# Optimization experiments

Hardware: AMD Instinct MI355X
Metric: run time of the kernel (lower is better)

## Reference

```python
import jax, jax.numpy as jnp
import numpy as np

STRIDE, PAD, DIL = 1, 1, 1


def setup_inputs() -> dict:
    key = jax.random.key(0)
    ks = jax.random.split(key, 5)
    N, Cin, H, W = 8, 256, 56, 56
    Cout, kh, kw = 256, 3, 3
    x = jax.random.normal(ks[0], (N, Cin, H, W), jnp.float32)
    offset = jax.random.normal(ks[1], (N, 2 * kh * kw, H, W), jnp.float32)
    mask = jax.random.uniform(ks[2], (N, kh * kw, H, W), jnp.float32)
    fan_in = Cin * kh * kw
    bound = float(np.sqrt(6.0 / fan_in))  # kaiming_uniform, relu gain
    weight = jax.random.uniform(ks[3], (Cout, Cin, kh, kw), jnp.float32, -bound, bound)
    bias = jnp.zeros((Cout,), jnp.float32)
    return {"x": x, "offset": offset, "mask": mask, "weight": weight, "bias": bias}


def _mdcn(x, offset, mask, weight, bias):
    N, Cin, H, W = x.shape
    Cout, _, kh, kw = weight.shape
    K = kh * kw
    Hout = (H + 2 * PAD - (DIL * (kh - 1) + 1)) // STRIDE + 1
    Wout = (W + 2 * PAD - (DIL * (kw - 1) + 1)) // STRIDE + 1
    # offset channels: [K, 2(y,x)] interleaved -> [N,K,2,Hout,Wout]
    off = offset.reshape(N, K, 2, Hout, Wout)
    dy, dx = off[:, :, 0], off[:, :, 1]
    ky = (jnp.arange(K) // kw) * DIL
    kx = (jnp.arange(K) % kw) * DIL
    base_y = jnp.arange(Hout) * STRIDE - PAD
    base_x = jnp.arange(Wout) * STRIDE - PAD
    py = dy + ky[None, :, None, None] + base_y[None, None, :, None]  # [N,K,Ho,Wo]
    px = dx + kx[None, :, None, None] + base_x[None, None, None, :]
    y0 = jnp.floor(py)
    x0 = jnp.floor(px)
    wy1 = py - y0
    wx1 = px - x0
    wy0 = 1.0 - wy1
    wx0 = 1.0 - wx1
    y0i = y0.astype(jnp.int32)
    x0i = x0.astype(jnp.int32)
    x_nhwc = jnp.transpose(x, (0, 2, 3, 1))  # [N,H,W,Cin]
    nidx = jnp.arange(N)[:, None, None, None]

    def gather(yi, xi):
        valid = (yi >= 0) & (yi < H) & (xi >= 0) & (xi < W)
        yc = jnp.clip(yi, 0, H - 1)
        xc = jnp.clip(xi, 0, W - 1)
        v = x_nhwc[nidx, yc, xc]  # [N,K,Ho,Wo,Cin]
        return v * valid[..., None].astype(x.dtype)

    v = (gather(y0i, x0i) * (wy0 * wx0)[..., None]
         + gather(y0i, x0i + 1) * (wy0 * wx1)[..., None]
         + gather(y0i + 1, x0i) * (wy1 * wx0)[..., None]
         + gather(y0i + 1, x0i + 1) * (wy1 * wx1)[..., None])
    v = v * mask.reshape(N, K, Hout, Wout)[..., None]
    wr = weight.reshape(Cout, Cin, K)
    out = jnp.einsum('nkhwc,ock->nohw', v, wr)
    return out + bias[None, :, None, None]


def reference(x, offset, mask, weight, bias):
    return _mdcn(x, offset, mask, weight, bias)
```

## Files before the change

### kernel.cpp

```cpp
#include <hip/hip_runtime.h>
#include <math.h>

#define H_ 56
#define W_ 56
#define CIN 256
#define COUT 256
#define NB 8
#define SPIX 3136
#define KG 2304
#define MTOT 25088
#define MT 128
#define NBLK 196
#define GUARD_PX 2048

typedef _Float16 v8hf __attribute__((ext_vector_type(8)));
typedef float    v4f  __attribute__((ext_vector_type(4)));

#define WAIT_VM(N)  do { asm volatile("s_waitcnt vmcnt(" #N ")" ::: "memory"); \
                         __builtin_amdgcn_sched_barrier(0); } while (0)
#define WAIT_LGKM0  do { asm volatile("s_waitcnt lgkmcnt(0)" ::: "memory"); \
                         __builtin_amdgcn_sched_barrier(0); } while (0)
#define BARR        do { asm volatile("s_barrier" ::: "memory"); } while (0)

__device__ __forceinline__ void async_copy16(const void* g, void* l) {
    __builtin_amdgcn_global_load_lds(
        (const __attribute__((address_space(1))) void*)g,
        (__attribute__((address_space(3))) void*)l, 16, 0, 0);
}

__global__ __launch_bounds__(256) void prep_xw(const float* __restrict__ x,
                                               const float* __restrict__ w,
                                               _Float16* __restrict__ xb,
                                               _Float16* __restrict__ bp) {
    __shared__ float tile[64][65];
    const int tid = threadIdx.x;
    if (blockIdx.z < 8) {
        const int n = blockIdx.z, c0 = blockIdx.y * 64, s0 = blockIdx.x * 64;
        const float* xp = x + (size_t)n * CIN * SPIX;
        _Float16* xo = xb + (size_t)n * SPIX * CIN;
#pragma unroll
        for (int i = 0; i < 16; ++i) {
            int idx = tid + i * 256;
            int cr = idx >> 6, sc = idx & 63;
            tile[cr][sc] = xp[(c0 + cr) * SPIX + s0 + sc];
        }
        __syncthreads();
#pragma unroll
        for (int i = 0; i < 16; ++i) {
            int idx = tid + i * 256;
            int sr = idx >> 6, cc = idx & 63;
            xo[(s0 + sr) * CIN + c0 + cc] = (_Float16)tile[cc][sr];
        }
    } else if (blockIdx.z == 8) {
        const int base = (blockIdx.y * 49 + blockIdx.x) * 256 + tid;
        for (int i = base; i < COUT * KG; i += 196 * 256) {
            const int o = i / KG;
            const int rem = i - o * KG;
            const int c = rem / 9;
            const int tap = rem - c * 9;
            bp[(size_t)o * KG + tap * 256 + c] = (_Float16)w[i];
        }
    } else {
        const int gtid = (blockIdx.y * 49 + blockIdx.x) * 256 + tid;
        v8hf* lo = (v8hf*)(xb - (size_t)GUARD_PX * CIN);
        v8hf* hi = (v8hf*)(xb + (size_t)NB * SPIX * CIN);
        const v8hf z = (v8hf)(_Float16)0.f;
        for (int i = gtid; i < 65536; i += 196 * 256) {
            lo[i] = z;
            hi[i] = z;
        }
    }
}

__device__ __forceinline__ void compute_params(
    const float* __restrict__ offs, const float* __restrict__ msk,
    int m0, int* sS, float4* sW, int tid)
{
    for (int idx = tid; idx < 9 * MT; idx += 512) {
        const int tl = idx >> 7, pl = idx & 127;
        const int pg = m0 + pl;
        const int n  = pg / SPIX;
        const int s  = pg - n * SPIX;
        const int h  = s / W_, w = s - h * W_;
        const int kY = tl / 3, kX = tl - kY * 3;
        const float dy = offs[n * (18 * SPIX) + (2 * tl) * SPIX + s];
        const float dx = offs[n * (18 * SPIX) + (2 * tl + 1) * SPIX + s];
        const float mk = msk[n * (9 * SPIX) + tl * SPIX + s];
        const float py = dy + (float)(kY + h - 1);
        const float px = dx + (float)(kX + w - 1);
        const float fy0 = floorf(py), fx0 = floorf(px);
        const int y0 = (int)fy0, x0 = (int)fx0;
        const float wy1 = py - fy0, wx1 = px - fx0;
        const float wy0 = 1.f - wy1, wx0 = 1.f - wx1;
        const bool yv0 = (y0 >= 0) & (y0 < H_);
        const bool yv1 = (y0 + 1 >= 0) & (y0 + 1 < H_);
        const bool xv0 = (x0 >= 0) & (x0 < W_);
        const bool xv1 = (x0 + 1 >= 0) & (x0 + 1 < W_);
        float4 wt;
        wt.x = (yv0 & xv0) ? wy0 * wx0 * mk : 0.f;
        wt.y = (yv0 & xv1) ? wy0 * wx1 * mk : 0.f;
        wt.z = (yv1 & xv0) ? wy1 * wx0 * mk : 0.f;
        wt.w = (yv1 & xv1) ? wy1 * wx1 * mk : 0.f;
        int base = n * SPIX + y0 * W_ + x0;
        base = min(max(base, -GUARD_PX), NB * SPIX - 58 + GUARD_PX);
        sS[idx] = base * CIN;
        sW[idx] = wt;
    }
}

__global__ __launch_bounds__(512, 2) void mdcn_fused6(
    const _Float16* __restrict__ xb,
    const float*    __restrict__ offs,
    const float*    __restrict__ msk,
    const _Float16* __restrict__ bp,
    const float*    __restrict__ bias,
    float*          __restrict__ out)
{
    __shared__ __align__(16) char smem[121344];
    int*    sS = (int*)(smem + 98304);
    float4* sW = (float4*)(smem + 102912);

    const int tid  = threadIdx.x;
    const int lane = tid & 63, wv = tid >> 6;
    const int wm = wv & 1, wn = wv >> 1;
    const int l15 = lane & 15, q = lane >> 4;

    const int xcd = blockIdx.x & 7, ib = blockIdx.x >> 3;
    const int wg  = (xcd < 4) ? xcd * 25 + ib : 100 + (xcd - 4) * 24 + ib;
    const int m0  = wg * MT;

    compute_params(offs, msk, m0, sS, sW, tid);

    v4f acc[4][4];
#pragma unroll
    for (int i = 0; i < 4; ++i)
#pragma unroll
        for (int j = 0; j < 4; ++j) acc[i][j] = (v4f)0.f;

    __syncthreads();

    const int pxl = tid >> 2, c2 = tid & 3;
    v8hf ga0, ga1, ga2, ga3, gb0, gb1, gb2, gb3;
    float4 cw;
    v8hf afr[2][4], bfr[2][4];

#define GATHER(E, KQ)                                                   \
    { const int b_ = sS[E] + ((KQ) << 6) + c2 * 8;                      \
      cw  = sW[E];                                                      \
      ga0 = *(const v8hf*)(xb + b_);                                    \
      ga1 = *(const v8hf*)(xb + b_ + 256);                              \
      ga2 = *(const v8hf*)(xb + b_ + 14336);                            \
      ga3 = *(const v8hf*)(xb + b_ + 14592);                            \
      gb0 = *(const v8hf*)(xb + b_ + 32);                               \
      gb1 = *(const v8hf*)(xb + b_ + 288);                              \
      gb2 = *(const v8hf*)(xb + b_ + 14368);                            \
      gb3 = *(const v8hf*)(xb + b_ + 14624); }

#define COMBINE_STORE(AP)                                               \
    { const _Float16 wx_ = (_Float16)cw.x, wy_ = (_Float16)cw.y;        \
      const _Float16 wz_ = (_Float16)cw.z, ww_ = (_Float16)cw.w;        \
      v8hf r0_ = ga0 * wx_ + ga1 * wy_ + ga2 * wz_ + ga3 * ww_;         \
      v8hf r1_ = gb0 * wx_ + gb1 * wy_ + gb2 * wz_ + gb3 * ww_;         \
      *(v8hf*)((AP) + pxl * 64 + (((c2)     ^ (pxl & 7)) << 3)) = r0_;  \
      *(v8hf*)((AP) + pxl * 64 + (((c2 + 4) ^ (pxl & 7)) << 3)) = r1_; }

#define STAGE_B(K0, LB)                                                 \
    do { _Pragma("unroll")                                              \
      for (int t = 0; t < 4; ++t) {                                     \
        const int brow = t * 64 + (wv << 3) + (lane >> 3);              \
        const int blc  = (lane & 7) ^ (brow & 7);                       \
        async_copy16(bp + (size_t)brow * KG + (K0) + blc * 8,           \
                     (LB) + ((t * 8 + wv) << 10)); } } while (0)

#define LOAD_FRAGS(AB, BB)                                              \
    { _Pragma("unroll")                                                 \
      for (int kf = 0; kf < 2; ++kf) {                                  \
        _Pragma("unroll")                                               \
        for (int mt = 0; mt < 4; ++mt) {                                \
          const int row = wm * 64 + mt * 16 + l15;                      \
          const int pch = (kf * 4 + q) ^ (row & 7);                     \
          afr[kf][mt] = *(const v8hf*)((_Float16*)(AB) + row * 64 + pch * 8); } \
        _Pragma("unroll")                                               \
        for (int nt = 0; nt < 4; ++nt) {                                \
          const int row = wn * 64 + nt * 16 + l15;                      \
          const int pch = (kf * 4 + q) ^ (row & 7);                     \
          bfr[kf][nt] = *(const v8hf*)((_Float16*)(BB) + row * 64 + pch * 8); } } }

#define MFMA_EXEC                                                       \
    { __builtin_amdgcn_s_setprio(1);                                    \
      _Pragma("unroll")                                                 \
      for (int kf = 0; kf < 2; ++kf)                                    \
        _Pragma("unroll")                                               \
        for (int mt = 0; mt < 4; ++mt)                                  \
          _Pragma("unroll")                                             \
          for (int nt = 0; nt < 4; ++nt)                                \
            acc[mt][nt] = __builtin_amdgcn_mfma_f32_16x16x32_f16(       \
                afr[kf][mt], bfr[kf][nt], acc[mt][nt], 0, 0, 0);        \
      __builtin_amdgcn_s_setprio(0); }

    GATHER(pxl, 0)
    COMBINE_STORE((_Float16*)smem)
    STAGE_B(0, smem + 32768);
    GATHER(pxl, 1)
    WAIT_LGKM0;
    WAIT_VM(8);
    BARR;

    char* ac = smem;          char* an = smem + 16384;
    char* bc = smem + 32768;  char* bn = smem + 65536;

#pragma unroll 1
    for (int ks = 0; ks < 36; ++ks) {
        LOAD_FRAGS(ac, bc);
        if (ks < 35) {
            STAGE_B((ks + 1) << 6, bn);
            WAIT_VM(4);
            COMBINE_STORE((_Float16*)an)
            if (ks < 34) {
                const int st = ks + 2;
                GATHER((st >> 2) * MT + pxl, st & 3)
            }
        }

        MFMA_EXEC;

        if (ks < 34) {
            WAIT_LGKM0;
            WAIT_VM(8);
            BARR;
        } else if (ks == 34) {
            WAIT_LGKM0;
            WAIT_VM(0);
            BARR;
        }
        char* t;
        t = ac; ac = an; an = t;
        t = bc; bc = bn; bn = t;
    }
#undef GATHER
#undef COMBINE_STORE
#undef STAGE_B
#undef LOAD_FRAGS
#undef MFMA_EXEC

    WAIT_LGKM0;
    BARR;
    float* epi = (float*)smem + wv * 1104;
    const int pg_l = m0 + wm * 64 + lane;
    const int n_l  = pg_l / SPIX;
    float* outp = out + (size_t)n_l * (COUT * SPIX) + (pg_l - n_l * SPIX);

#pragma unroll
    for (int nt = 0; nt < 4; ++nt) {
        const float bv = bias[wn * 64 + nt * 16 + l15];
#pragma unroll
        for (int mt = 0; mt < 4; ++mt)
#pragma unroll
            for (int r = 0; r < 4; ++r)
                epi[(mt * 16 + q * 4 + r) * 17 + l15] = acc[mt][nt][r] + bv;
#pragma unroll
        for (int oc = 0; oc < 16; ++oc)
            outp[(size_t)(wn * 64 + nt * 16 + oc) * SPIX] = epi[lane * 17 + oc];
    }
}

#define BM 64
#define BN 64
#define BKF 32
#define AST 68
#define BST 68
#define CST 65
__global__ __launch_bounds__(256) void mdcn_fallback(
    const float* __restrict__ xs, const float* __restrict__ offs,
    const float* __restrict__ msk, const float* __restrict__ wraw,
    const float* __restrict__ bias, float* __restrict__ out)
{
    __shared__ float smem[BKF * AST + BKF * BST];
    __shared__ int   sBase[4][BM];
    __shared__ float sWgt[4][BM];
    float (*At)[AST] = (float (*)[AST])smem;
    float (*Bt)[BST] = (float (*)[BST])(smem + BKF * AST);
    float (*Cs)[CST] = (float (*)[CST])smem;
    const int tid = threadIdx.x;
    const int m0 = blockIdx.x * BM;
    const int o0 = blockIdx.y * BN;
    const int n  = m0 / SPIX;
    const int s0 = m0 - n * SPIX;
    const int tx = tid & 15, ty = tid >> 4;
    float acc[4][4] = {};
    for (int k = 0; k < 9; ++k) {
        if (tid < BM) {
            const int s = s0 + tid;
            const int h = s / W_;
            const int w = s - h * W_;
            const int kY = k / 3, kX = k - kY * 3;
            const float dy = offs[(size_t)n * (18 * SPIX) + (size_t)(2 * k) * SPIX + s];
            const float dx = offs[(size_t)n * (18 * SPIX) + (size_t)(2 * k + 1) * SPIX + s];
            const float mk = msk[(size_t)n * (9 * SPIX) + (size_t)k * SPIX + s];
            const float py = dy + (float)(kY + h - 1);
            const float px = dx + (float)(kX + w - 1);
            const float fy0 = floorf(py), fx0 = floorf(px);
            const int y0 = (int)fy0, x0 = (int)fx0;
            const float wy1 = py - fy0, wx1 = px - fx0;
            const float wy0 = 1.0f - wy1, wx0 = 1.0f - wx1;
#pragma unroll
            for (int t = 0; t < 4; ++t) {
                const int yi = y0 + (t >> 1), xi = x0 + (t & 1);
                const bool valid = (yi >= 0) & (yi < H_) & (xi >= 0) & (xi < W_);
                const int yc = min(max(yi, 0), H_ - 1);
                const int xc = min(max(xi, 0), W_ - 1);
                float wt = ((t >> 1) ? wy1 : wy0) * ((t & 1) ? wx1 : wx0) * mk;
                sBase[t][tid] = n * (CIN * SPIX) + yc * W_ + xc;
                sWgt[t][tid] = valid ? wt : 0.0f;
            }
        }
        __syncthreads();
        for (int c0 = 0; c0 < CIN; c0 += BKF) {
#pragma unroll
            for (int i = 0; i < 8; ++i) {
                int idx = tid + i * 256;
                int row = idx >> 5, cc = idx & 31;
                int ce = (c0 + cc) * SPIX;
                At[cc][row] = sWgt[0][row] * xs[sBase[0][row] + ce]
                            + sWgt[1][row] * xs[sBase[1][row] + ce]
                            + sWgt[2][row] * xs[sBase[2][row] + ce]
                            + sWgt[3][row] * xs[sBase[3][row] + ce];
            }
#pragma unroll
            for (int i = 0; i < 8; ++i) {
                int idx = tid + i * 256;
                int kf = idx >> 6, o = idx & 63;
                Bt[kf][o] = wraw[(size_t)(o0 + o) * KG + (c0 + kf) * 9 + k];
            }
            __syncthreads();
#pragma unroll
            for (int kf = 0; kf < BKF; ++kf) {
                const float4 a = *(const float4*)&At[kf][ty * 4];
                const float4 b = *(const float4*)&Bt[kf][tx * 4];
                acc[0][0] = fmaf(a.x, b.x, acc[0][0]); acc[0][1] = fmaf(a.x, b.y, acc[0][1]);
                acc[0][2] = fmaf(a.x, b.z, acc[0][2]); acc[0][3] = fmaf(a.x, b.w, acc[0][3]);
                acc[1][0] = fmaf(a.y, b.x, acc[1][0]); acc[1][1] = fmaf(a.y, b.y, acc[1][1]);
                acc[1][2] = fmaf(a.y, b.z, acc[1][2]); acc[1][3] = fmaf(a.y, b.w, acc[1][3]);
                acc[2][0] = fmaf(a.z, b.x, acc[2][0]); acc[2][1] = fmaf(a.z, b.y, acc[2][1]);
                acc[2][2] = fmaf(a.z, b.z, acc[2][2]); acc[2][3] = fmaf(a.z, b.w, acc[2][3]);
                acc[3][0] = fmaf(a.w, b.x, acc[3][0]); acc[3][1] = fmaf(a.w, b.y, acc[3][1]);
                acc[3][2] = fmaf(a.w, b.z, acc[3][2]); acc[3][3] = fmaf(a.w, b.w, acc[3][3]);
            }
            __syncthreads();
        }
    }
#pragma unroll
    for (int i = 0; i < 4; ++i)
#pragma unroll
        for (int j = 0; j < 4; ++j)
            Cs[ty * 4 + i][tx * 4 + j] = acc[i][j] + bias[o0 + tx * 4 + j];
    __syncthreads();
    const int pix = tid & 63, ob = tid >> 6;
    float* outp = out + (size_t)n * COUT * SPIX + s0 + pix;
#pragma unroll
    for (int r = 0; r < 16; ++r) {
        int o = r * 4 + ob;
        outp[(size_t)(o0 + o) * SPIX] = Cs[pix][o];
    }
}

extern "C" void kernel_launch(void* const* d_in, const int* in_sizes, int n_in,
                              void* d_out, int out_size, void* d_ws, size_t ws_size,
                              hipStream_t stream) {
    const float* x    = (const float*)d_in[0];
    const float* offs = (const float*)d_in[1];
    const float* msk  = (const float*)d_in[2];
    const float* w    = (const float*)d_in[3];
    const float* bias = (const float*)d_in[4];
    float* out = (float*)d_out;

    const size_t GUARD_B  = (size_t)GUARD_PX * CIN * sizeof(_Float16);
    const size_t xb_bytes = (size_t)NB * SPIX * CIN * sizeof(_Float16);
    const size_t bp_bytes = (size_t)KG * COUT * sizeof(_Float16);
    const size_t need     = GUARD_B + xb_bytes + GUARD_B + bp_bytes;

    if (ws_size >= need) {
        _Float16* xb = (_Float16*)((char*)d_ws + GUARD_B);
        _Float16* bp = (_Float16*)((char*)d_ws + GUARD_B + xb_bytes + GUARD_B);
        prep_xw<<<dim3(49, 4, 10), 256, 0, stream>>>(x, w, xb, bp);
        mdcn_fused6<<<dim3(NBLK), 512, 0, stream>>>(xb, offs, msk, bp, bias, out);
    } else {
        mdcn_fallback<<<dim3(MTOT / BM, COUT / BN), 256, 0, stream>>>(
            x, offs, msk, w, bias, out);
    }
}
```

Before: 143.3 us.

## Halve M tile, stream B fragments directly into registers, drop LDS B staging

The fused kernel moves from 128-pixel tiles with 512 threads to 64-pixel tiles with 256 threads and 392 blocks, which shrinks LDS from about 121KB to about 28KB. Each wave now owns 64 output channels and loads its B (weight) fragments straight from global memory into double-buffered registers, replacing the async global-to-LDS copies and the LDS fragment reads. The main loop is unrolled by two to alternate the A and B buffers. This aims for more blocks in flight and less LDS traffic, at the cost of each block re-reading the full weight matrix from global/L2 and more register pressure.

```diff
diff --git a/kernel.cpp b/kernel.cpp
--- a/kernel.cpp
+++ b/kernel.cpp
@@ -9,8 +9,8 @@
 #define SPIX 3136
 #define KG 2304
 #define MTOT 25088
-#define MT 128
-#define NBLK 196
+#define MT 64
+#define NBLK2 392
 #define GUARD_PX 2048
 
 typedef _Float16 v8hf __attribute__((ext_vector_type(8)));
@@ -21,12 +21,6 @@
 #define WAIT_LGKM0  do { asm volatile("s_waitcnt lgkmcnt(0)" ::: "memory"); \
                          __builtin_amdgcn_sched_barrier(0); } while (0)
 #define BARR        do { asm volatile("s_barrier" ::: "memory"); } while (0)
-
-__device__ __forceinline__ void async_copy16(const void* g, void* l) {
-    __builtin_amdgcn_global_load_lds(
-        (const __attribute__((address_space(1))) void*)g,
-        (__attribute__((address_space(3))) void*)l, 16, 0, 0);
-}
 
 __global__ __launch_bounds__(256) void prep_xw(const float* __restrict__ x,
                                                const float* __restrict__ w,
@@ -76,8 +70,8 @@
     const float* __restrict__ offs, const float* __restrict__ msk,
     int m0, int* sS, float4* sW, int tid)
 {
-    for (int idx = tid; idx < 9 * MT; idx += 512) {
-        const int tl = idx >> 7, pl = idx & 127;
+    for (int idx = tid; idx < 9 * MT; idx += 256) {
+        const int tl = idx >> 6, pl = idx & 63;
         const int pg = m0 + pl;
         const int n  = pg / SPIX;
         const int s  = pg - n * SPIX;
@@ -108,7 +102,7 @@
     }
 }
 
-__global__ __launch_bounds__(512, 2) void mdcn_fused6(
+__global__ __launch_bounds__(256, 2) void mdcn_fused8(
     const _Float16* __restrict__ xb,
     const float*    __restrict__ offs,
     const float*    __restrict__ msk,
@@ -116,18 +110,18 @@
     const float*    __restrict__ bias,
     float*          __restrict__ out)
 {
-    __shared__ __align__(16) char smem[121344];
-    int*    sS = (int*)(smem + 98304);
-    float4* sW = (float4*)(smem + 102912);
+    __shared__ __align__(16) char smem[28160];
+    _Float16* A0 = (_Float16*)smem;
+    _Float16* A1 = (_Float16*)(smem + 8192);
+    int*      sS = (int*)(smem + 16384);
+    float4*   sW = (float4*)(smem + 18688);
 
     const int tid  = threadIdx.x;
     const int lane = tid & 63, wv = tid >> 6;
-    const int wm = wv & 1, wn = wv >> 1;
     const int l15 = lane & 15, q = lane >> 4;
 
-    const int xcd = blockIdx.x & 7, ib = blockIdx.x >> 3;
-    const int wg  = (xcd < 4) ? xcd * 25 + ib : 100 + (xcd - 4) * 24 + ib;
-    const int m0  = wg * MT;
+    const int wg = (blockIdx.x & 7) * 49 + (blockIdx.x >> 3);
+    const int m0 = wg * MT;
 
     compute_params(offs, msk, m0, sS, sW, tid);
 
@@ -142,11 +136,13 @@
     const int pxl = tid >> 2, c2 = tid & 3;
     v8hf ga0, ga1, ga2, ga3, gb0, gb1, gb2, gb3;
     float4 cw;
-    v8hf afr[2][4], bfr[2][4];
+    v8hf afr[2][4];
+    v8hf B0r[8], B1r[8];
 
 #define GATHER(E, KQ)                                                   \
-    { const int b_ = sS[E] + ((KQ) << 6) + c2 * 8;                      \
-      cw  = sW[E];                                                      \
+    { const int e_ = (E);                                               \
+      const int b_ = sS[e_] + ((KQ) << 6) + c2 * 8;                     \
+      cw  = sW[e_];                                                     \
       ga0 = *(const v8hf*)(xb + b_);                                    \
       ga1 = *(const v8hf*)(xb + b_ + 256);                              \
       ga2 = *(const v8hf*)(xb + b_ + 14336);                            \
@@ -164,29 +160,24 @@
       *(v8hf*)((AP) + pxl * 64 + (((c2)     ^ (pxl & 7)) << 3)) = r0_;  \
       *(v8hf*)((AP) + pxl * 64 + (((c2 + 4) ^ (pxl & 7)) << 3)) = r1_; }
 
-#define STAGE_B(K0, LB)                                                 \
-    do { _Pragma("unroll")                                              \
-      for (int t = 0; t < 4; ++t) {                                     \
-        const int brow = t * 64 + (wv << 3) + (lane >> 3);              \
-        const int blc  = (lane & 7) ^ (brow & 7);                       \
-        async_copy16(bp + (size_t)brow * KG + (K0) + blc * 8,           \
-                     (LB) + ((t * 8 + wv) << 10)); } } while (0)
-
-#define LOAD_FRAGS(AB, BB)                                              \
+#define ISSUE_B(KS, BR)                                                 \
     { _Pragma("unroll")                                                 \
-      for (int kf = 0; kf < 2; ++kf) {                                  \
+      for (int i = 0; i < 8; ++i) {                                     \
+        const int kf_ = i >> 2, nt_ = i & 3;                            \
+        BR[i] = *(const v8hf*)(bp                                       \
+            + (size_t)(wv * 64 + nt_ * 16 + l15) * KG                   \
+            + (KS) * 64 + (kf_ * 4 + q) * 8); } }
+
+#define LOAD_AFR(AB)                                                    \
+    { _Pragma("unroll")                                                 \
+      for (int kf = 0; kf < 2; ++kf)                                    \
         _Pragma("unroll")                                               \
         for (int mt = 0; mt < 4; ++mt) {                                \
-          const int row = wm * 64 + mt * 16 + l15;                      \
+          const int row = mt * 16 + l15;                                \
           const int pch = (kf * 4 + q) ^ (row & 7);                     \
-          afr[kf][mt] = *(const v8hf*)((_Float16*)(AB) + row * 64 + pch * 8); } \
-        _Pragma("unroll")                                               \
-        for (int nt = 0; nt < 4; ++nt) {                                \
-          const int row = wn * 64 + nt * 16 + l15;                      \
-          const int pch = (kf * 4 + q) ^ (row & 7);                     \
-          bfr[kf][nt] = *(const v8hf*)((_Float16*)(BB) + row * 64 + pch * 8); } } }
-
-#define MFMA_EXEC                                                       \
+          afr[kf][mt] = *(const v8hf*)((AB) + row * 64 + pch * 8); } }
+
+#define MFMA_EXEC(BR)                                                   \
     { __builtin_amdgcn_s_setprio(1);                                    \
       _Pragma("unroll")                                                 \
       for (int kf = 0; kf < 2; ++kf)                                    \
@@ -195,64 +186,69 @@
           _Pragma("unroll")                                             \
           for (int nt = 0; nt < 4; ++nt)                                \
             acc[mt][nt] = __builtin_amdgcn_mfma_f32_16x16x32_f16(       \
-                afr[kf][mt], bfr[kf][nt], acc[mt][nt], 0, 0, 0);        \
+                afr[kf][mt], BR[kf * 4 + nt], acc[mt][nt], 0, 0, 0);    \
       __builtin_amdgcn_s_setprio(0); }
 
+    ISSUE_B(0, B0r);
     GATHER(pxl, 0)
-    COMBINE_STORE((_Float16*)smem)
-    STAGE_B(0, smem + 32768);
+    WAIT_VM(0);
+    COMBINE_STORE(A0)
     GATHER(pxl, 1)
+    ISSUE_B(1, B1r);
     WAIT_LGKM0;
+    BARR;
+
+#pragma unroll 1
+    for (int k2 = 0; k2 < 17; ++k2) {
+        const int e = k2 * 2;
+        LOAD_AFR(A0);
+        WAIT_VM(8);
+        COMBINE_STORE(A1)
+        GATHER(((e + 2) >> 2) * MT + pxl, (e + 2) & 3)
+        WAIT_VM(8);
+        MFMA_EXEC(B0r);
+        ISSUE_B(e + 2, B0r);
+        WAIT_LGKM0;
+        BARR;
+
+        const int o = e + 1;
+        LOAD_AFR(A1);
+        WAIT_VM(8);
+        COMBINE_STORE(A0)
+        GATHER(((o + 2) >> 2) * MT + pxl, (o + 2) & 3)
+        WAIT_VM(8);
+        MFMA_EXEC(B1r);
+        ISSUE_B(o + 2, B1r);
+        WAIT_LGKM0;
+        BARR;
+    }
+
+    LOAD_AFR(A0);
     WAIT_VM(8);
+    COMBINE_STORE(A1)
+    WAIT_VM(0);
+    MFMA_EXEC(B0r);
+    WAIT_LGKM0;
     BARR;
-
-    char* ac = smem;          char* an = smem + 16384;
-    char* bc = smem + 32768;  char* bn = smem + 65536;
-
-#pragma unroll 1
-    for (int ks = 0; ks < 36; ++ks) {
-        LOAD_FRAGS(ac, bc);
-        if (ks < 35) {
-            STAGE_B((ks + 1) << 6, bn);
-            WAIT_VM(4);
-            COMBINE_STORE((_Float16*)an)
-            if (ks < 34) {
-                const int st = ks + 2;
-                GATHER((st >> 2) * MT + pxl, st & 3)
-            }
-        }
-
-        MFMA_EXEC;
-
-        if (ks < 34) {
-            WAIT_LGKM0;
-            WAIT_VM(8);
-            BARR;
-        } else if (ks == 34) {
-            WAIT_LGKM0;
-            WAIT_VM(0);
-            BARR;
-        }
-        char* t;
-        t = ac; ac = an; an = t;
-        t = bc; bc = bn; bn = t;
-    }
+    LOAD_AFR(A1);
+    MFMA_EXEC(B1r);
+
 #undef GATHER
 #undef COMBINE_STORE
-#undef STAGE_B
-#undef LOAD_FRAGS
+#undef ISSUE_B
+#undef LOAD_AFR
 #undef MFMA_EXEC
 
     WAIT_LGKM0;
     BARR;
     float* epi = (float*)smem + wv * 1104;
-    const int pg_l = m0 + wm * 64 + lane;
+    const int pg_l = m0 + lane;
     const int n_l  = pg_l / SPIX;
     float* outp = out + (size_t)n_l * (COUT * SPIX) + (pg_l - n_l * SPIX);
 
 #pragma unroll
     for (int nt = 0; nt < 4; ++nt) {
-        const float bv = bias[wn * 64 + nt * 16 + l15];
+        const float bv = bias[wv * 64 + nt * 16 + l15];
 #pragma unroll
         for (int mt = 0; mt < 4; ++mt)
 #pragma unroll
@@ -260,7 +256,7 @@
                 epi[(mt * 16 + q * 4 + r) * 17 + l15] = acc[mt][nt][r] + bv;
 #pragma unroll
         for (int oc = 0; oc < 16; ++oc)
-            outp[(size_t)(wn * 64 + nt * 16 + oc) * SPIX] = epi[lane * 17 + oc];
+            outp[(size_t)(wv * 64 + nt * 16 + oc) * SPIX] = epi[lane * 17 + oc];
     }
 }
 
@@ -383,7 +379,7 @@
         _Float16* xb = (_Float16*)((char*)d_ws + GUARD_B);
         _Float16* bp = (_Float16*)((char*)d_ws + GUARD_B + xb_bytes + GUARD_B);
         prep_xw<<<dim3(49, 4, 10), 256, 0, stream>>>(x, w, xb, bp);
-        mdcn_fused6<<<dim3(NBLK), 512, 0, stream>>>(xb, offs, msk, bp, bias, out);
+        mdcn_fused8<<<dim3(NBLK2), 256, 0, stream>>>(xb, offs, msk, bp, bias, out);
     } else {
         mdcn_fallback<<<dim3(MTOT / BM, COUT / BN), 256, 0, stream>>>(
             x, offs, msk, w, bias, out);
```

Measured after the change: 171.8 us. 1.2x slower.

## Warp-specialize fused deformable conv into producer gather and consumer MFMA waves

Applied to the files above, without the earlier changes.

Splits the 8 waves of each block into 4 producer waves, which gather the bilinear samples, combine them, and stage weight tiles into LDS, and 4 consumer waves that run only the MFMA loop. Each consumer wave now covers a 64x128 output tile instead of 64x64. The aim is to overlap the irregular gather latency with tensor-core math rather than interleaving both in every wave. In exchange, each producer wave issues twice as many gather loads, consumer waves hold twice as many accumulator registers, and MFMA throughput per block is limited to half the waves.

```diff
diff --git a/kernel.cpp b/kernel.cpp
--- a/kernel.cpp
+++ b/kernel.cpp
@@ -108,7 +108,7 @@
     }
 }
 
-__global__ __launch_bounds__(512, 2) void mdcn_fused6(
+__global__ __launch_bounds__(512, 2) void mdcn_fused9(
     const _Float16* __restrict__ xb,
     const float*    __restrict__ offs,
     const float*    __restrict__ msk,
@@ -122,7 +122,6 @@
 
     const int tid  = threadIdx.x;
     const int lane = tid & 63, wv = tid >> 6;
-    const int wm = wv & 1, wn = wv >> 1;
     const int l15 = lane & 15, q = lane >> 4;
 
     const int xcd = blockIdx.x & 7, ib = blockIdx.x >> 3;
@@ -130,137 +129,158 @@
     const int m0  = wg * MT;
 
     compute_params(offs, msk, m0, sS, sW, tid);
-
-    v4f acc[4][4];
-#pragma unroll
-    for (int i = 0; i < 4; ++i)
-#pragma unroll
-        for (int j = 0; j < 4; ++j) acc[i][j] = (v4f)0.f;
-
     __syncthreads();
 
-    const int pxl = tid >> 2, c2 = tid & 3;
-    v8hf ga0, ga1, ga2, ga3, gb0, gb1, gb2, gb3;
-    float4 cw;
-    v8hf afr[2][4], bfr[2][4];
-
-#define GATHER(E, KQ)                                                   \
-    { const int b_ = sS[E] + ((KQ) << 6) + c2 * 8;                      \
-      cw  = sW[E];                                                      \
-      ga0 = *(const v8hf*)(xb + b_);                                    \
-      ga1 = *(const v8hf*)(xb + b_ + 256);                              \
-      ga2 = *(const v8hf*)(xb + b_ + 14336);                            \
-      ga3 = *(const v8hf*)(xb + b_ + 14592);                            \
-      gb0 = *(const v8hf*)(xb + b_ + 32);                               \
-      gb1 = *(const v8hf*)(xb + b_ + 288);                              \
-      gb2 = *(const v8hf*)(xb + b_ + 14368);                            \
-      gb3 = *(const v8hf*)(xb + b_ + 14624); }
-
-#define COMBINE_STORE(AP)                                               \
-    { const _Float16 wx_ = (_Float16)cw.x, wy_ = (_Float16)cw.y;        \
-      const _Float16 wz_ = (_Float16)cw.z, ww_ = (_Float16)cw.w;        \
-      v8hf r0_ = ga0 * wx_ + ga1 * wy_ + ga2 * wz_ + ga3 * ww_;         \
-      v8hf r1_ = gb0 * wx_ + gb1 * wy_ + gb2 * wz_ + gb3 * ww_;         \
-      *(v8hf*)((AP) + pxl * 64 + (((c2)     ^ (pxl & 7)) << 3)) = r0_;  \
-      *(v8hf*)((AP) + pxl * 64 + (((c2 + 4) ^ (pxl & 7)) << 3)) = r1_; }
-
-#define STAGE_B(K0, LB)                                                 \
-    do { _Pragma("unroll")                                              \
-      for (int t = 0; t < 4; ++t) {                                     \
-        const int brow = t * 64 + (wv << 3) + (lane >> 3);              \
-        const int blc  = (lane & 7) ^ (brow & 7);                       \
-        async_copy16(bp + (size_t)brow * KG + (K0) + blc * 8,           \
-                     (LB) + ((t * 8 + wv) << 10)); } } while (0)
-
-#define LOAD_FRAGS(AB, BB)                                              \
-    { _Pragma("unroll")                                                 \
-      for (int kf = 0; kf < 2; ++kf) {                                  \
-        _Pragma("unroll")                                               \
-        for (int mt = 0; mt < 4; ++mt) {                                \
-          const int row = wm * 64 + mt * 16 + l15;                      \
-          const int pch = (kf * 4 + q) ^ (row & 7);                     \
-          afr[kf][mt] = *(const v8hf*)((_Float16*)(AB) + row * 64 + pch * 8); } \
-        _Pragma("unroll")                                               \
-        for (int nt = 0; nt < 4; ++nt) {                                \
-          const int row = wn * 64 + nt * 16 + l15;                      \
-          const int pch = (kf * 4 + q) ^ (row & 7);                     \
-          bfr[kf][nt] = *(const v8hf*)((_Float16*)(BB) + row * 64 + pch * 8); } } }
-
-#define MFMA_EXEC                                                       \
-    { __builtin_amdgcn_s_setprio(1);                                    \
-      _Pragma("unroll")                                                 \
-      for (int kf = 0; kf < 2; ++kf)                                    \
-        _Pragma("unroll")                                               \
-        for (int mt = 0; mt < 4; ++mt)                                  \
-          _Pragma("unroll")                                             \
-          for (int nt = 0; nt < 4; ++nt)                                \
-            acc[mt][nt] = __builtin_amdgcn_mfma_f32_16x16x32_f16(       \
-                afr[kf][mt], bfr[kf][nt], acc[mt][nt], 0, 0, 0);        \
-      __builtin_amdgcn_s_setprio(0); }
-
-    GATHER(pxl, 0)
-    COMBINE_STORE((_Float16*)smem)
-    STAGE_B(0, smem + 32768);
-    GATHER(pxl, 1)
-    WAIT_LGKM0;
-    WAIT_VM(8);
-    BARR;
-
-    char* ac = smem;          char* an = smem + 16384;
-    char* bc = smem + 32768;  char* bn = smem + 65536;
-
+    if (wv < 4) {
+        const int p2 = tid >> 2, c2 = tid & 3;
+        v8hf gA[8], gB[8];
+        float4 cwA, cwB;
+
+#define GATHER16(TAP, KQ)                                               \
+        { const int e0_ = (TAP) * MT + p2;                              \
+          const int b0_ = sS[e0_]      + ((KQ) << 6) + c2 * 8;          \
+          const int b1_ = sS[e0_ + 64] + ((KQ) << 6) + c2 * 8;          \
+          cwA = sW[e0_]; cwB = sW[e0_ + 64];                            \
+          gA[0] = *(const v8hf*)(xb + b0_);                             \
+          gA[1] = *(const v8hf*)(xb + b0_ + 256);                       \
+          gA[2] = *(const v8hf*)(xb + b0_ + 14336);                     \
+          gA[3] = *(const v8hf*)(xb + b0_ + 14592);                     \
+          gA[4] = *(const v8hf*)(xb + b0_ + 32);                        \
+          gA[5] = *(const v8hf*)(xb + b0_ + 288);                       \
+          gA[6] = *(const v8hf*)(xb + b0_ + 14368);                     \
+          gA[7] = *(const v8hf*)(xb + b0_ + 14624);                     \
+          gB[0] = *(const v8hf*)(xb + b1_);                             \
+          gB[1] = *(const v8hf*)(xb + b1_ + 256);                       \
+          gB[2] = *(const v8hf*)(xb + b1_ + 14336);                     \
+          gB[3] = *(const v8hf*)(xb + b1_ + 14592);                     \
+          gB[4] = *(const v8hf*)(xb + b1_ + 32);                        \
+          gB[5] = *(const v8hf*)(xb + b1_ + 288);                       \
+          gB[6] = *(const v8hf*)(xb + b1_ + 14368);                     \
+          gB[7] = *(const v8hf*)(xb + b1_ + 14624); }
+
+#define COMBINE16(AP)                                                   \
+        { const _Float16 ax_ = (_Float16)cwA.x, ay_ = (_Float16)cwA.y;  \
+          const _Float16 az_ = (_Float16)cwA.z, aw_ = (_Float16)cwA.w;  \
+          const _Float16 bx_ = (_Float16)cwB.x, by_ = (_Float16)cwB.y;  \
+          const _Float16 bz_ = (_Float16)cwB.z, bw_ = (_Float16)cwB.w;  \
+          v8hf rA0 = gA[0]*ax_ + gA[1]*ay_ + gA[2]*az_ + gA[3]*aw_;     \
+          v8hf rA1 = gA[4]*ax_ + gA[5]*ay_ + gA[6]*az_ + gA[7]*aw_;     \
+          v8hf rB0 = gB[0]*bx_ + gB[1]*by_ + gB[2]*bz_ + gB[3]*bw_;     \
+          v8hf rB1 = gB[4]*bx_ + gB[5]*by_ + gB[6]*bz_ + gB[7]*bw_;     \
+          _Float16* ap_ = (_Float16*)(AP);                              \
+          *(v8hf*)(ap_ + p2 * 64        + (((c2)     ^ (p2 & 7)) << 3)) = rA0; \
+          *(v8hf*)(ap_ + p2 * 64        + (((c2 + 4) ^ (p2 & 7)) << 3)) = rA1; \
+          *(v8hf*)(ap_ + (p2 + 64) * 64 + (((c2)     ^ (p2 & 7)) << 3)) = rB0; \
+          *(v8hf*)(ap_ + (p2 + 64) * 64 + (((c2 + 4) ^ (p2 & 7)) << 3)) = rB1; }
+
+#define STAGE_B8(K0, LB)                                                \
+        do { _Pragma("unroll")                                          \
+          for (int t = 0; t < 8; ++t) {                                 \
+            const int brow = t * 32 + (wv << 3) + (lane >> 3);          \
+            const int blc  = (lane & 7) ^ (brow & 7);                   \
+            async_copy16(bp + (size_t)brow * KG + (K0) + blc * 8,       \
+                         (LB) + ((t * 4 + wv) << 10)); } } while (0)
+
+        GATHER16(0, 0)
+        STAGE_B8(0, smem + 32768);
+        WAIT_VM(8);
+        COMBINE16(smem)
+        GATHER16(0, 1)
+        WAIT_VM(16);
+        WAIT_LGKM0;
+        BARR;
+
+        char* pa = smem + 16384;
+        char* pb = smem + 65536;
 #pragma unroll 1
-    for (int ks = 0; ks < 36; ++ks) {
-        LOAD_FRAGS(ac, bc);
-        if (ks < 35) {
-            STAGE_B((ks + 1) << 6, bn);
-            WAIT_VM(4);
-            COMBINE_STORE((_Float16*)an)
-            if (ks < 34) {
-                const int st = ks + 2;
-                GATHER((st >> 2) * MT + pxl, st & 3)
-            }
-        }
-
-        MFMA_EXEC;
-
-        if (ks < 34) {
+        for (int ks = 0; ks < 36; ++ks) {
+            if (ks < 35) {
+                STAGE_B8((ks + 1) << 6, pb);
+                WAIT_VM(8);
+                COMBINE16(pa)
+                if (ks < 34) {
+                    const int st = ks + 2;
+                    GATHER16(st >> 2, st & 3)
+                    WAIT_VM(16);
+                } else {
+                    WAIT_VM(0);
+                }
+                WAIT_LGKM0;
+            }
+            BARR;
+            pa = (char*)((size_t)smem + 16384 - ((size_t)pa - (size_t)smem));
+            pb = (char*)((size_t)smem + 32768 + 65536 + 32768
+                         - ((size_t)pb - (size_t)smem) - 32768);
+        }
+        BARR;
+#undef GATHER16
+#undef COMBINE16
+#undef STAGE_B8
+    } else {
+        const int cw_id = wv - 4;
+        const int wm = cw_id & 1, wn = cw_id >> 1;
+
+        v4f acc[4][8];
+#pragma unroll
+        for (int i = 0; i < 4; ++i)
+#pragma unroll
+            for (int j = 0; j < 8; ++j) acc[i][j] = (v4f)0.f;
+
+        BARR;
+
+        char* ca = smem;
+        char* cb = smem + 32768;
+#pragma unroll 1
+        for (int ks = 0; ks < 36; ++ks) {
+#pragma unroll
+            for (int kf = 0; kf < 2; ++kf) {
+                v8hf afr[4], bfr[8];
+#pragma unroll
+                for (int mt = 0; mt < 4; ++mt) {
+                    const int row = wm * 64 + mt * 16 + l15;
+                    const int pch = (kf * 4 + q) ^ (row & 7);
+                    afr[mt] = *(const v8hf*)((_Float16*)ca + row * 64 + pch * 8);
+                }
+#pragma unroll
+                for (int nt = 0; nt < 8; ++nt) {
+                    const int row = wn * 128 + nt * 16 + l15;
+                    const int pch = (kf * 4 + q) ^ (row & 7);
+                    bfr[nt] = *(const v8hf*)((_Float16*)cb + row * 64 + pch * 8);
+                }
+                __builtin_amdgcn_s_setprio(1);
+#pragma unroll
+                for (int mt = 0; mt < 4; ++mt)
+#pragma unroll
+                    for (int nt = 0; nt < 8; ++nt)
+                        acc[mt][nt] = __builtin_amdgcn_mfma_f32_16x16x32_f16(
+                            afr[mt], bfr[nt], acc[mt][nt], 0, 0, 0);
+                __builtin_amdgcn_s_setprio(0);
+            }
             WAIT_LGKM0;
-            WAIT_VM(8);
             BARR;
-        } else if (ks == 34) {
-            WAIT_LGKM0;
-            WAIT_VM(0);
-            BARR;
-        }
-        char* t;
-        t = ac; ac = an; an = t;
-        t = bc; bc = bn; bn = t;
-    }
-#undef GATHER
-#undef COMBINE_STORE
-#undef STAGE_B
-#undef LOAD_FRAGS
-#undef MFMA_EXEC
-
-    WAIT_LGKM0;
-    BARR;
-    float* epi = (float*)smem + wv * 1104;
-    const int pg_l = m0 + wm * 64 + lane;
-    const int n_l  = pg_l / SPIX;
-    float* outp = out + (size_t)n_l * (COUT * SPIX) + (pg_l - n_l * SPIX);
-
-#pragma unroll
-    for (int nt = 0; nt < 4; ++nt) {
-        const float bv = bias[wn * 64 + nt * 16 + l15];
-#pragma unroll
-        for (int mt = 0; mt < 4; ++mt)
-#pragma unroll
-            for (int r = 0; r < 4; ++r)
-                epi[(mt * 16 + q * 4 + r) * 17 + l15] = acc[mt][nt][r] + bv;
-#pragma unroll
-        for (int oc = 0; oc < 16; ++oc)
-            outp[(size_t)(wn * 64 + nt * 16 + oc) * SPIX] = epi[lane * 17 + oc];
+            ca = (char*)((size_t)smem + 16384 - ((size_t)ca - (size_t)smem));
+            cb = (char*)((size_t)smem + 32768 + 65536 + 32768
+                         - ((size_t)cb - (size_t)smem) - 32768);
+        }
+        BARR;
+
+        float* epi = (float*)smem + cw_id * 1104;
+        const int pg_l = m0 + wm * 64 + lane;
+        const int n_l  = pg_l / SPIX;
+        float* outp = out + (size_t)n_l * (COUT * SPIX) + (pg_l - n_l * SPIX);
+
+#pragma unroll
+        for (int nt = 0; nt < 8; ++nt) {
+            const float bv = bias[wn * 128 + nt * 16 + l15];
+#pragma unroll
+            for (int mt = 0; mt < 4; ++mt)
+#pragma unroll
+                for (int r = 0; r < 4; ++r)
+                    epi[(mt * 16 + q * 4 + r) * 17 + l15] = acc[mt][nt][r] + bv;
+#pragma unroll
+            for (int oc = 0; oc < 16; ++oc)
+                outp[(size_t)(wn * 128 + nt * 16 + oc) * SPIX] = epi[lane * 17 + oc];
+        }
     }
 }
 
@@ -383,7 +403,7 @@
         _Float16* xb = (_Float16*)((char*)d_ws + GUARD_B);
         _Float16* bp = (_Float16*)((char*)d_ws + GUARD_B + xb_bytes + GUARD_B);
         prep_xw<<<dim3(49, 4, 10), 256, 0, stream>>>(x, w, xb, bp);
-        mdcn_fused6<<<dim3(NBLK), 512, 0, stream>>>(xb, offs, msk, bp, bias, out);
+        mdcn_fused9<<<dim3(NBLK), 512, 0, stream>>>(xb, offs, msk, bp, bias, out);
     } else {
         mdcn_fallback<<<dim3(MTOT / BM, COUT / BN), 256, 0, stream>>>(
             x, offs, msk, w, bias, out);
```

Result: slower. 167.9 us (+17.2%).

## Split reduction over K across two blocks with atomic accumulation

Applied to the files above, without the earlier changes.

Splits the 2304-long reduction into two halves handled by a second grid dimension, each block covering 36 steps of K=32 instead of 64, which halves shared memory per block and lets more blocks fit per CU. Partial results are combined with float atomicAdd into an output zeroed beforehand with a memset, and only the first split adds the bias. This doubles the block count (392 versus 196) to fill more CUs, at the cost of atomic traffic, an extra memset and twice the epilogue writes.

```diff
diff --git a/kernel.cpp b/kernel.cpp
--- a/kernel.cpp
+++ b/kernel.cpp
@@ -74,18 +74,19 @@
 
 __device__ __forceinline__ void compute_params(
     const float* __restrict__ offs, const float* __restrict__ msk,
-    int m0, int* sS, float4* sW, int tid)
+    int m0, int t0, int* sS, float4* sW, int tid)
 {
-    for (int idx = tid; idx < 9 * MT; idx += 512) {
-        const int tl = idx >> 7, pl = idx & 127;
+    for (int idx = tid; idx < 5 * MT; idx += 512) {
+        const int lt = idx >> 7, pl = idx & 127;
+        const int tap = t0 + lt;
         const int pg = m0 + pl;
         const int n  = pg / SPIX;
         const int s  = pg - n * SPIX;
         const int h  = s / W_, w = s - h * W_;
-        const int kY = tl / 3, kX = tl - kY * 3;
-        const float dy = offs[n * (18 * SPIX) + (2 * tl) * SPIX + s];
-        const float dx = offs[n * (18 * SPIX) + (2 * tl + 1) * SPIX + s];
-        const float mk = msk[n * (9 * SPIX) + tl * SPIX + s];
+        const int kY = tap / 3, kX = tap - kY * 3;
+        const float dy = offs[n * (18 * SPIX) + (2 * tap) * SPIX + s];
+        const float dx = offs[n * (18 * SPIX) + (2 * tap + 1) * SPIX + s];
+        const float mk = msk[n * (9 * SPIX) + tap * SPIX + s];
         const float py = dy + (float)(kY + h - 1);
         const float px = dx + (float)(kX + w - 1);
         const float fy0 = floorf(py), fx0 = floorf(px);
@@ -108,7 +109,7 @@
     }
 }
 
-__global__ __launch_bounds__(512, 2) void mdcn_fused6(
+__global__ __launch_bounds__(512, 4) void mdcn_fused10(
     const _Float16* __restrict__ xb,
     const float*    __restrict__ offs,
     const float*    __restrict__ msk,
@@ -116,20 +117,22 @@
     const float*    __restrict__ bias,
     float*          __restrict__ out)
 {
-    __shared__ __align__(16) char smem[121344];
-    int*    sS = (int*)(smem + 98304);
-    float4* sW = (float4*)(smem + 102912);
+    __shared__ __align__(16) char smem[61952];
+    int*    sS = (int*)(smem + 49152);
+    float4* sW = (float4*)(smem + 51712);
 
     const int tid  = threadIdx.x;
     const int lane = tid & 63, wv = tid >> 6;
     const int wm = wv & 1, wn = wv >> 1;
     const int l15 = lane & 15, q = lane >> 4;
+    const int kz  = blockIdx.y;
+    const int gs0 = kz * 36;
 
     const int xcd = blockIdx.x & 7, ib = blockIdx.x >> 3;
     const int wg  = (xcd < 4) ? xcd * 25 + ib : 100 + (xcd - 4) * 24 + ib;
     const int m0  = wg * MT;
 
-    compute_params(offs, msk, m0, sS, sW, tid);
+    compute_params(offs, msk, m0, kz * 4, sS, sW, tid);
 
     v4f acc[4][4];
 #pragma unroll
@@ -140,85 +143,76 @@
     __syncthreads();
 
     const int pxl = tid >> 2, c2 = tid & 3;
-    v8hf ga0, ga1, ga2, ga3, gb0, gb1, gb2, gb3;
+    v8hf g0, g1, g2, g3;
     float4 cw;
-    v8hf afr[2][4], bfr[2][4];
-
-#define GATHER(E, KQ)                                                   \
-    { const int b_ = sS[E] + ((KQ) << 6) + c2 * 8;                      \
-      cw  = sW[E];                                                      \
-      ga0 = *(const v8hf*)(xb + b_);                                    \
-      ga1 = *(const v8hf*)(xb + b_ + 256);                              \
-      ga2 = *(const v8hf*)(xb + b_ + 14336);                            \
-      ga3 = *(const v8hf*)(xb + b_ + 14592);                            \
-      gb0 = *(const v8hf*)(xb + b_ + 32);                               \
-      gb1 = *(const v8hf*)(xb + b_ + 288);                              \
-      gb2 = *(const v8hf*)(xb + b_ + 14368);                            \
-      gb3 = *(const v8hf*)(xb + b_ + 14624); }
+    v8hf afr[4], bfr[4];
+
+#define GATHER(E, CH)                                                   \
+    { const int b_ = sS[E] + ((CH) << 5) + c2 * 8;                      \
+      cw = sW[E];                                                       \
+      g0 = *(const v8hf*)(xb + b_);                                     \
+      g1 = *(const v8hf*)(xb + b_ + 256);                               \
+      g2 = *(const v8hf*)(xb + b_ + 14336);                             \
+      g3 = *(const v8hf*)(xb + b_ + 14592); }
 
 #define COMBINE_STORE(AP)                                               \
     { const _Float16 wx_ = (_Float16)cw.x, wy_ = (_Float16)cw.y;        \
       const _Float16 wz_ = (_Float16)cw.z, ww_ = (_Float16)cw.w;        \
-      v8hf r0_ = ga0 * wx_ + ga1 * wy_ + ga2 * wz_ + ga3 * ww_;         \
-      v8hf r1_ = gb0 * wx_ + gb1 * wy_ + gb2 * wz_ + gb3 * ww_;         \
-      *(v8hf*)((AP) + pxl * 64 + (((c2)     ^ (pxl & 7)) << 3)) = r0_;  \
-      *(v8hf*)((AP) + pxl * 64 + (((c2 + 4) ^ (pxl & 7)) << 3)) = r1_; }
-
-#define STAGE_B(K0, LB)                                                 \
+      v8hf r_ = g0 * wx_ + g1 * wy_ + g2 * wz_ + g3 * ww_;              \
+      *(v8hf*)((_Float16*)(AP) + pxl * 32 + (((c2) ^ (pxl & 3)) << 3)) = r_; }
+
+#define STAGE_B(GS, LB)                                                 \
     do { _Pragma("unroll")                                              \
-      for (int t = 0; t < 4; ++t) {                                     \
-        const int brow = t * 64 + (wv << 3) + (lane >> 3);              \
-        const int blc  = (lane & 7) ^ (brow & 7);                       \
-        async_copy16(bp + (size_t)brow * KG + (K0) + blc * 8,           \
-                     (LB) + ((t * 8 + wv) << 10)); } } while (0)
+      for (int t = 0; t < 2; ++t) {                                     \
+        const int brow = (wv * 2 + t) * 16 + (lane >> 2);               \
+        const int blc  = (lane & 3) ^ (brow & 3);                       \
+        async_copy16(bp + (size_t)brow * KG + (size_t)(GS) * 32 + blc * 8, \
+                     (LB) + ((wv * 2 + t) << 10)); } } while (0)
 
 #define LOAD_FRAGS(AB, BB)                                              \
     { _Pragma("unroll")                                                 \
-      for (int kf = 0; kf < 2; ++kf) {                                  \
-        _Pragma("unroll")                                               \
-        for (int mt = 0; mt < 4; ++mt) {                                \
-          const int row = wm * 64 + mt * 16 + l15;                      \
-          const int pch = (kf * 4 + q) ^ (row & 7);                     \
-          afr[kf][mt] = *(const v8hf*)((_Float16*)(AB) + row * 64 + pch * 8); } \
-        _Pragma("unroll")                                               \
-        for (int nt = 0; nt < 4; ++nt) {                                \
-          const int row = wn * 64 + nt * 16 + l15;                      \
-          const int pch = (kf * 4 + q) ^ (row & 7);                     \
-          bfr[kf][nt] = *(const v8hf*)((_Float16*)(BB) + row * 64 + pch * 8); } } }
+      for (int mt = 0; mt < 4; ++mt) {                                  \
+        const int row = wm * 64 + mt * 16 + l15;                        \
+        const int ch  = q ^ (row & 3);                                  \
+        afr[mt] = *(const v8hf*)((_Float16*)(AB) + row * 32 + ch * 8); }\
+      _Pragma("unroll")                                                 \
+      for (int nt = 0; nt < 4; ++nt) {                                  \
+        const int row = wn * 64 + nt * 16 + l15;                        \
+        const int ch  = q ^ (row & 3);                                  \
+        bfr[nt] = *(const v8hf*)((_Float16*)(BB) + row * 32 + ch * 8); } }
 
 #define MFMA_EXEC                                                       \
     { __builtin_amdgcn_s_setprio(1);                                    \
       _Pragma("unroll")                                                 \
-      for (int kf = 0; kf < 2; ++kf)                                    \
+      for (int mt = 0; mt < 4; ++mt)                                    \
         _Pragma("unroll")                                               \
-        for (int mt = 0; mt < 4; ++mt)                                  \
-          _Pragma("unroll")                                             \
-          for (int nt = 0; nt < 4; ++nt)                                \
-            acc[mt][nt] = __builtin_amdgcn_mfma_f32_16x16x32_f16(       \
-                afr[kf][mt], bfr[kf][nt], acc[mt][nt], 0, 0, 0);        \
+        for (int nt = 0; nt < 4; ++nt)                                  \
+          acc[mt][nt] = __builtin_amdgcn_mfma_f32_16x16x32_f16(         \
+              afr[mt], bfr[nt], acc[mt][nt], 0, 0, 0);                  \
       __builtin_amdgcn_s_setprio(0); }
 
-    GATHER(pxl, 0)
-    COMBINE_STORE((_Float16*)smem)
-    STAGE_B(0, smem + 32768);
-    GATHER(pxl, 1)
+    GATHER(pxl, gs0 & 7)
+    COMBINE_STORE(smem)
+    STAGE_B(gs0, smem + 16384);
+    { const int s1 = gs0 + 1;
+      GATHER(((s1 >> 3) - kz * 4) * MT + pxl, s1 & 7) }
     WAIT_LGKM0;
-    WAIT_VM(8);
+    WAIT_VM(4);
     BARR;
 
-    char* ac = smem;          char* an = smem + 16384;
-    char* bc = smem + 32768;  char* bn = smem + 65536;
+    char* ac = smem;          char* an = smem + 8192;
+    char* bc = smem + 16384;  char* bn = smem + 32768;
 
 #pragma unroll 1
     for (int ks = 0; ks < 36; ++ks) {
         LOAD_FRAGS(ac, bc);
         if (ks < 35) {
-            STAGE_B((ks + 1) << 6, bn);
-            WAIT_VM(4);
-            COMBINE_STORE((_Float16*)an)
+            STAGE_B(gs0 + ks + 1, bn);
+            WAIT_VM(2);
+            COMBINE_STORE(an)
             if (ks < 34) {
-                const int st = ks + 2;
-                GATHER((st >> 2) * MT + pxl, st & 3)
+                const int st = gs0 + ks + 2;
+                GATHER(((st >> 3) - kz * 4) * MT + pxl, st & 7)
             }
         }
 
@@ -226,7 +220,7 @@
 
         if (ks < 34) {
             WAIT_LGKM0;
-            WAIT_VM(8);
+            WAIT_VM(4);
             BARR;
         } else if (ks == 34) {
             WAIT_LGKM0;
@@ -252,7 +246,7 @@
 
 #pragma unroll
     for (int nt = 0; nt < 4; ++nt) {
-        const float bv = bias[wn * 64 + nt * 16 + l15];
+        const float bv = (kz == 0) ? bias[wn * 64 + nt * 16 + l15] : 0.0f;
 #pragma unroll
         for (int mt = 0; mt < 4; ++mt)
 #pragma unroll
@@ -260,7 +254,8 @@
                 epi[(mt * 16 + q * 4 + r) * 17 + l15] = acc[mt][nt][r] + bv;
 #pragma unroll
         for (int oc = 0; oc < 16; ++oc)
-            outp[(size_t)(wn * 64 + nt * 16 + oc) * SPIX] = epi[lane * 17 + oc];
+            atomicAdd(&outp[(size_t)(wn * 64 + nt * 16 + oc) * SPIX],
+                      epi[lane * 17 + oc]);
     }
 }
 
@@ -382,8 +377,9 @@
     if (ws_size >= need) {
         _Float16* xb = (_Float16*)((char*)d_ws + GUARD_B);
         _Float16* bp = (_Float16*)((char*)d_ws + GUARD_B + xb_bytes + GUARD_B);
+        hipMemsetAsync(out, 0, (size_t)out_size * sizeof(float), stream);
         prep_xw<<<dim3(49, 4, 10), 256, 0, stream>>>(x, w, xb, bp);
-        mdcn_fused6<<<dim3(NBLK), 512, 0, stream>>>(xb, offs, msk, bp, bias, out);
+        mdcn_fused10<<<dim3(NBLK, 2), 512, 0, stream>>>(xb, offs, msk, bp, bias, out);
     } else {
         mdcn_fallback<<<dim3(MTOT / BM, COUT / BN), 256, 0, stream>>>(
             x, offs, msk, w, bias, out);
```

Measured after the change: 257.5 us. 79.7% more time.
